# Performance work log

Hardware: AMD Instinct MI355X
Metric: run time of the kernel (lower is better)

## Reference

```python
import jax, jax.numpy as jnp
import numpy as np

EPS = 1e-6
NUM_HEADS = 24

def _rmsnorm(x, w):
    # x: [..., D], fp32 math as in FluxRMSNorm
    xf = x.astype(jnp.float32)
    inv = jax.lax.rsqrt(jnp.mean(xf * xf, axis=-1, keepdims=True) + EPS)
    return w * (xf * inv).astype(x.dtype)

def setup_inputs() -> dict:
    key = jax.random.key(0)
    ks = jax.random.split(key, 4)
    B, N, H = 1, 2048, 3072
    D = H // NUM_HEADS
    s_in = 1.0 / np.sqrt(H)
    return {
        "x": jax.random.normal(ks[0], (B, N, H), jnp.float32),
        "Wqkv": jax.random.normal(ks[1], (H, 3 * H), jnp.float32) * s_in,
        "b_qkv": jnp.zeros((3 * H,), jnp.float32),
        "Wproj": jax.random.normal(ks[2], (H, H), jnp.float32) * s_in,
        "q_norm_w": jnp.ones((D,), jnp.float32),
        "k_norm_w": jnp.ones((D,), jnp.float32),
    }

def reference(x, Wqkv, b_qkv, Wproj, q_norm_w, k_norm_w):
    B, N, hidden = x.shape
    nh = NUM_HEADS
    hd = hidden // nh
    scale = hd ** (-0.5)
    qkv = (x @ Wqkv + b_qkv).reshape(B, N, 3, nh, hd)
    q, k, v = qkv[:, :, 0], qkv[:, :, 1], qkv[:, :, 2]  # [B,N,nh,hd]
    q = _rmsnorm(q, q_norm_w)
    k = _rmsnorm(k, k_norm_w)
    # scores: [B,nh,N,N]
    scores = jnp.einsum('bqhd,bkhd->bhqk', q, k) * scale
    attn = jax.nn.softmax(scores, axis=-1)
    out = jnp.einsum('bhqk,bkhd->bqhd', attn, v).reshape(B, N, hidden)
    return out @ Wproj
```

## Files before the change

### kernel.cpp

```cpp
#include <hip/hip_runtime.h>
#include <hip/hip_bf16.h>

using bf16 = __hip_bfloat16;
typedef __attribute__((ext_vector_type(8))) short short8;
typedef __attribute__((ext_vector_type(4))) float f32x4;
typedef unsigned long long ull;

static constexpr int SEQ  = 2048;
static constexpr int HID  = 3072;
static constexpr int NH   = 24;
static constexpr int HD   = 128;
static constexpr int QKVN = 9216;

__device__ __forceinline__ f32x4 mfma_16x16x32(short8 a, short8 b, f32x4 c) {
  return __builtin_amdgcn_mfma_f32_16x16x32_bf16(a, b, c, 0, 0, 0);
}

#define GLOAD_LDS16(g, l) __builtin_amdgcn_global_load_lds(                 \
    (const __attribute__((address_space(1))) void*)(g),                    \
    (__attribute__((address_space(3))) void*)(l), 16, 0, 0)

typedef __attribute__((address_space(3))) const unsigned char lds_cchar;

__device__ __forceinline__ unsigned pack_bf16(float lo, float hi) {
  bf16 l = __float2bfloat16(lo), h = __float2bfloat16(hi);
  return (unsigned)*(unsigned short*)&l | ((unsigned)*(unsigned short*)&h << 16);
}

__global__ __launch_bounds__(256)
void cvt_f32_bf16_vec(const float* __restrict__ src, bf16* __restrict__ dst, int n4) {
  int i = blockIdx.x * 256 + threadIdx.x;
  if (i >= n4) return;
  float4 v = ((const float4*)src)[i];
  ushort4 o;
  bf16 t0 = __float2bfloat16(v.x); o.x = *(unsigned short*)&t0;
  bf16 t1 = __float2bfloat16(v.y); o.y = *(unsigned short*)&t1;
  bf16 t2 = __float2bfloat16(v.z); o.z = *(unsigned short*)&t2;
  bf16 t3 = __float2bfloat16(v.w); o.w = *(unsigned short*)&t3;
  ((ushort4*)dst)[i] = o;
}

__global__ __launch_bounds__(256)
void transpose_cvt64(const float* __restrict__ src, bf16* __restrict__ dst, int R, int C) {
  __shared__ float tile[32][65];
  const int c0 = blockIdx.x * 64, r0 = blockIdx.y * 32;
  const int lc = threadIdx.x & 63, lt = threadIdx.x >> 6;
  #pragma unroll
  for (int i = 0; i < 8; ++i)
    tile[lt + i * 4][lc] = src[(size_t)(r0 + lt + i * 4) * C + c0 + lc];
  __syncthreads();
  const int u = threadIdx.x & 15, dr = threadIdx.x >> 4;
  #pragma unroll
  for (int j = 0; j < 4; ++j) {
    const int cc = dr + j * 16;
    bf16 x0 = __float2bfloat16(tile[u * 2][cc]);
    bf16 x1 = __float2bfloat16(tile[u * 2 + 1][cc]);
    ushort2 o;
    o.x = *(unsigned short*)&x0; o.y = *(unsigned short*)&x1;
    *(ushort2*)&dst[(size_t)(c0 + cc) * R + r0 + u * 2] = o;
  }
}

template<int BIAS>
__global__ __launch_bounds__(768, 3)
void gemm12w(const bf16* __restrict__ A, const bf16* __restrict__ BT,
             const float* __restrict__ bias, bf16* __restrict__ Cout,
             int M, int N, int K) {
  __shared__ __align__(16) bf16 Asb[2][256 * 64];
  __shared__ __align__(16) bf16 Bsb[2][288 * 64];

  const int tid  = threadIdx.x;
  const int lane = tid & 63;
  const int wid  = tid >> 6;
  const int wm   = wid / 6;
  const int wn   = wid % 6;
  const int lr   = lane & 15;
  const int lg   = lane >> 4;

  const int xcd = blockIdx.x & 7;
  const int q   = blockIdx.x >> 3;
  const int bm  = (q & 7) * 256;
  const int bn  = (xcd * 4 + (q >> 3)) * 288;

  const int lrow = lane >> 3;
  const int csrc = ((lane & 7) ^ lrow) * 8;
  const bf16* Abase = A  + (size_t)(bm + lrow) * K + csrc;
  const bf16* Bbase = BT + (size_t)(bn + lrow) * K + csrc;

#define STG12(b, u, i) do {                                                       \
    const int L_ = wid + 12 * (i);                                                \
    if (L_ < 32)      GLOAD_LDS16(Abase + (size_t)(8 * L_) * K + (size_t)(u) * 64,\
                                  &Asb[b][L_ * 512]);                             \
    else if (L_ < 68) GLOAD_LDS16(Bbase + (size_t)(8 * (L_ - 32)) * K + (size_t)(u) * 64, \
                                  &Bsb[b][(L_ - 32) * 512]);                      \
  } while (0)
#define RA12(b, m, kk) (*(const short8*)(&Asb[b][(wm * 128 + (m) * 16 + lr) * 64 \
                          + ((((kk) * 4 + lg)) ^ (lr & 7)) * 8]))
#define RB12(b, n, kk) (*(const short8*)(&Bsb[b][(wn * 48 + (n) * 16 + lr) * 64 \
                          + ((((kk) * 4 + lg)) ^ (lr & 7)) * 8]))

  f32x4 acc[8][3] = {};
  const int NT = K >> 6;

  #pragma unroll
  for (int i = 0; i < 6; ++i) STG12(0, 0, i);

  for (int t = 0; t < NT; ++t) {
    const int c = t & 1, nc = c ^ 1;
    const bool pf = (t + 1) < NT;
    short8 a[4], b[3];

    asm volatile("s_waitcnt vmcnt(0)" ::: "memory");
    __builtin_amdgcn_s_barrier();

    if (pf) {
      STG12(nc, t + 1, 0); STG12(nc, t + 1, 1); STG12(nc, t + 1, 2);
      STG12(nc, t + 1, 3); STG12(nc, t + 1, 4); STG12(nc, t + 1, 5);
    }
    __builtin_amdgcn_sched_barrier(0);

    b[0] = RB12(c, 0, 0); b[1] = RB12(c, 1, 0); b[2] = RB12(c, 2, 0);
    a[0] = RA12(c, 0, 0); a[1] = RA12(c, 1, 0); a[2] = RA12(c, 2, 0); a[3] = RA12(c, 3, 0);
    #pragma unroll
    for (int n = 0; n < 3; ++n)
      #pragma unroll
      for (int m = 0; m < 4; ++m) acc[m][n] = mfma_16x16x32(a[m], b[n], acc[m][n]);

    a[0] = RA12(c, 4, 0); a[1] = RA12(c, 5, 0); a[2] = RA12(c, 6, 0); a[3] = RA12(c, 7, 0);
    #pragma unroll
    for (int n = 0; n < 3; ++n)
      #pragma unroll
      for (int m = 0; m < 4; ++m) acc[4 + m][n] = mfma_16x16x32(a[m], b[n], acc[4 + m][n]);

    b[0] = RB12(c, 0, 1); b[1] = RB12(c, 1, 1); b[2] = RB12(c, 2, 1);
    a[0] = RA12(c, 0, 1); a[1] = RA12(c, 1, 1); a[2] = RA12(c, 2, 1); a[3] = RA12(c, 3, 1);
    #pragma unroll
    for (int n = 0; n < 3; ++n)
      #pragma unroll
      for (int m = 0; m < 4; ++m) acc[m][n] = mfma_16x16x32(a[m], b[n], acc[m][n]);

    a[0] = RA12(c, 4, 1); a[1] = RA12(c, 5, 1); a[2] = RA12(c, 6, 1); a[3] = RA12(c, 7, 1);
    #pragma unroll
    for (int n = 0; n < 3; ++n)
      #pragma unroll
      for (int m = 0; m < 4; ++m) acc[4 + m][n] = mfma_16x16x32(a[m], b[n], acc[4 + m][n]);
  }
#undef STG12
#undef RA12
#undef RB12

  const int row0 = bm + wm * 128 + lg * 4;
  const int col0 = bn + wn * 48 + lr;
  #pragma unroll
  for (int n = 0; n < 3; ++n) {
    const int col = col0 + n * 16;
    const float bv = BIAS ? bias[col] : 0.0f;
    #pragma unroll
    for (int m = 0; m < 8; ++m)
      #pragma unroll
      for (int r = 0; r < 4; ++r)
        Cout[(size_t)(row0 + m * 16 + r) * N + col] = __float2bfloat16(acc[m][n][r] + bv);
  }
}

__global__ __launch_bounds__(512, 2)
void gemm8w(const bf16* __restrict__ A, const bf16* __restrict__ BT,
            float* __restrict__ Cout, int M, int N, int K) {
  __shared__ __align__(16) bf16 Asb[2][128 * 64];
  __shared__ __align__(16) bf16 Bsb[2][192 * 64];

  const int tid  = threadIdx.x;
  const int lane = tid & 63;
  const int wid  = tid >> 6;
  const int wm   = wid >> 2;
  const int wn   = wid & 3;
  const int lr   = lane & 15;
  const int lg   = lane >> 4;

  const int xcd = blockIdx.x & 7;
  const int q   = blockIdx.x >> 3;
  const int bm  = (q >> 1) * 128;
  const int bn  = (xcd * 2 + (q & 1)) * 192;

  const int lrow = lane >> 3;
  const int csrc = ((lane & 7) ^ lrow) * 8;
  const bf16* Abase = A  + (size_t)(bm + lrow) * K + csrc;
  const bf16* Bbase = BT + (size_t)(bn + lrow) * K + csrc;

#define STG8(b, u, i) do {                                                        \
    const int L_ = wid + 8 * (i);                                                 \
    if (L_ < 16)      GLOAD_LDS16(Abase + (size_t)(8 * L_) * K + (size_t)(u) * 64,\
                                  &Asb[b][L_ * 512]);                             \
    else              GLOAD_LDS16(Bbase + (size_t)(8 * (L_ - 16)) * K + (size_t)(u) * 64, \
                                  &Bsb[b][(L_ - 16) * 512]);                      \
  } while (0)
#define RA8(b, m, kk) (*(const short8*)(&Asb[b][(wm * 64 + (m) * 16 + lr) * 64 \
                          + ((((kk) * 4 + lg)) ^ (lr & 7)) * 8]))
#define RB8(b, n, kk) (*(const short8*)(&Bsb[b][(wn * 48 + (n) * 16 + lr) * 64 \
                          + ((((kk) * 4 + lg)) ^ (lr & 7)) * 8]))

  f32x4 acc[4][3] = {};
  const int NT = K >> 6;

  #pragma unroll
  for (int i = 0; i < 5; ++i) STG8(0, 0, i);

  for (int t = 0; t < NT; ++t) {
    const int c = t & 1, nc = c ^ 1;
    const bool pf = (t + 1) < NT;
    short8 a[4], b[3];

    asm volatile("s_waitcnt vmcnt(0)" ::: "memory");
    __builtin_amdgcn_s_barrier();

    if (pf) {
      STG8(nc, t + 1, 0); STG8(nc, t + 1, 1); STG8(nc, t + 1, 2);
      STG8(nc, t + 1, 3); STG8(nc, t + 1, 4);
    }
    __builtin_amdgcn_sched_barrier(0);

    b[0] = RB8(c, 0, 0); b[1] = RB8(c, 1, 0); b[2] = RB8(c, 2, 0);
    a[0] = RA8(c, 0, 0); a[1] = RA8(c, 1, 0); a[2] = RA8(c, 2, 0); a[3] = RA8(c, 3, 0);
    #pragma unroll
    for (int n = 0; n < 3; ++n)
      #pragma unroll
      for (int m = 0; m < 4; ++m) acc[m][n] = mfma_16x16x32(a[m], b[n], acc[m][n]);

    b[0] = RB8(c, 0, 1); b[1] = RB8(c, 1, 1); b[2] = RB8(c, 2, 1);
    a[0] = RA8(c, 0, 1); a[1] = RA8(c, 1, 1); a[2] = RA8(c, 2, 1); a[3] = RA8(c, 3, 1);
    #pragma unroll
    for (int n = 0; n < 3; ++n)
      #pragma unroll
      for (int m = 0; m < 4; ++m) acc[m][n] = mfma_16x16x32(a[m], b[n], acc[m][n]);
  }
#undef STG8
#undef RA8
#undef RB8

  const int row0 = bm + wm * 64 + lg * 4;
  const int col0 = bn + wn * 48 + lr;
  #pragma unroll
  for (int n = 0; n < 3; ++n) {
    const int col = col0 + n * 16;
    #pragma unroll
    for (int m = 0; m < 4; ++m)
      #pragma unroll
      for (int r = 0; r < 4; ++r)
        Cout[(size_t)(row0 + m * 16 + r) * N + col] = acc[m][n][r];
  }
}

__global__ __launch_bounds__(256)
void rmsnorm_qk(bf16* __restrict__ qkv, const float* __restrict__ qw,
                const float* __restrict__ kw) {
  const int row  = blockIdx.x * 4 + (threadIdx.x >> 6);
  const int lane = threadIdx.x & 63;
  const int token = row / 48;
  const int rem   = row - token * 48;
  const int which = rem / 24;
  const int head  = rem - which * 24;
  bf16* p = qkv + (long)token * QKVN + which * HID + head * HD;
  const float a = __bfloat162float(p[lane * 2]);
  const float b = __bfloat162float(p[lane * 2 + 1]);
  float ss = a * a + b * b;
  #pragma unroll
  for (int mask = 32; mask >= 1; mask >>= 1) ss += __shfl_xor(ss, mask);
  const float inv = rsqrtf(ss * (1.0f / 128.0f) + 1e-6f);
  const float* w = which ? kw : qw;
  p[lane * 2]     = __float2bfloat16(a * inv * w[lane * 2]);
  p[lane * 2 + 1] = __float2bfloat16(b * inv * w[lane * 2 + 1]);
}

__global__ __launch_bounds__(256, 3)
void attn_kernel(const bf16* __restrict__ qkv, bf16* __restrict__ ctx) {
  const int head = blockIdx.y;
  const int qb   = blockIdx.x;
  const int tid  = threadIdx.x;
  const int lane = tid & 63;
  const int wid  = tid >> 6;
  const int lr   = lane & 15;
  const int lg   = lane >> 4;

  __shared__ __align__(16) unsigned char Ksb[64 * 256];
  __shared__ __align__(16) unsigned char Vsb[128 * 128];
  __shared__ __align__(16) unsigned short Ps[4][16 * 72];

  const int qrow0 = qb * 64 + wid * 16;
  short8 qf[4];
  #pragma unroll
  for (int kt = 0; kt < 4; ++kt)
    qf[kt] = *(const short8*)(qkv + (long)(qrow0 + lr) * QKVN + head * HD + kt * 32 + lg * 8);

  f32x4 oacc[8] = {};
  float mrun = -1e30f, lsum = 0.0f;

  const float scale = 0.088388347648318447f;

  const int stok = tid >> 4;
  const int sdc  = tid & 15;

  short8 kreg[4], vreg[4];
  #pragma unroll
  for (int j = 0; j < 4; ++j) {
    const int tok = stok + (j & 1) * 16 + (j >> 1) * 32;
    kreg[j] = *(const short8*)(qkv + (long)tok * QKVN + HID     + head * HD + sdc * 8);
    vreg[j] = *(const short8*)(qkv + (long)tok * QKVN + 2 * HID + head * HD + sdc * 8);
  }

  for (int t = 0; t < SEQ / 64; ++t) {
    __syncthreads();
    #pragma unroll
    for (int j = 0; j < 4; ++j) {
      const int tok = stok + (j & 1) * 16 + (j >> 1) * 32;
      const int dc  = sdc;
      *(short8*)(Ksb + ((tok * 256 + dc * 16) ^ ((tok & 7) << 4))) = kreg[j];
      const int dg = dc >> 1, h = dc & 1, kg = tok >> 2, kr = tok & 3;
      const int pos = (kg & 8) | ((kg & 1) << 2) | ((kg >> 1) & 3);
      *(short8*)(Vsb + (dg * 16 + pos) * 128 + kr * 32 + h * 16) = vreg[j];
    }
    __syncthreads();

    if (t + 1 < SEQ / 64) {
      const int kv1 = (t + 1) * 64;
      #pragma unroll
      for (int j = 0; j < 4; ++j) {
        const int tok = kv1 + stok + (j & 1) * 16 + (j >> 1) * 32;
        kreg[j] = *(const short8*)(qkv + (long)tok * QKVN + HID     + head * HD + sdc * 8);
        vreg[j] = *(const short8*)(qkv + (long)tok * QKVN + 2 * HID + head * HD + sdc * 8);
      }
      __builtin_amdgcn_sched_barrier(0);
    }

    f32x4 st[4];
    __builtin_amdgcn_s_setprio(1);
    #pragma unroll
    for (int ct = 0; ct < 4; ++ct) {
      f32x4 a = {};
      #pragma unroll
      for (int kt = 0; kt < 4; ++kt) {
        short8 kb = *(const short8*)(Ksb +
            ((((ct * 16 + lr) * 256) + kt * 64 + lg * 16) ^ ((lr & 7) << 4)));
        a = mfma_16x16x32(kb, qf[kt], a);
      }
      st[ct] = a;
    }
    __builtin_amdgcn_s_setprio(0);

    float pm = st[0][0];
    #pragma unroll
    for (int ct = 0; ct < 4; ++ct)
      #pragma unroll
      for (int r = 0; r < 4; ++r) pm = fmaxf(pm, st[ct][r]);
    pm *= scale;
    pm = fmaxf(pm, __shfl_xor(pm, 16));
    pm = fmaxf(pm, __shfl_xor(pm, 32));

    if (!__all(pm <= mrun + 8.0f)) {
      const float mnew = fmaxf(mrun, pm);
      const float corr = __expf(mrun - mnew);
      mrun = mnew;
      lsum *= corr;
      #pragma unroll
      for (int r = 0; r < 4; ++r) {
        const float cr = __shfl(corr, lg * 4 + r);
        #pragma unroll
        for (int dt = 0; dt < 8; ++dt) oacc[dt][r] *= cr;
      }
    }

    float ps = 0.0f;
    #pragma unroll
    for (int ct = 0; ct < 4; ++ct) {
      const float p0 = __expf(st[ct][0] * scale - mrun);
      const float p1 = __expf(st[ct][1] * scale - mrun);
      const float p2 = __expf(st[ct][2] * scale - mrun);
      const float p3 = __expf(st[ct][3] * scale - mrun);
      ps += (p0 + p1) + (p2 + p3);
      uint2 w;
      w.x = pack_bf16(p0, p1);
      w.y = pack_bf16(p2, p3);
      *(uint2*)&Ps[wid][lr * 72 + ct * 16 + lg * 4] = w;
    }
    lsum += ps;

    short8 pa[2];
    #pragma unroll
    for (int kt = 0; kt < 2; ++kt)
      pa[kt] = *(const short8*)&Ps[wid][lr * 72 + kt * 32 + lg * 8];

    lds_cchar* vb0 = (lds_cchar*)Vsb + lane * 8;
    __builtin_amdgcn_s_setprio(1);
    #pragma unroll
    for (int dt = 0; dt < 8; ++dt) {
      lds_cchar* pd = vb0 + dt * 2048;
      ull r0, r1, r2, r3;
      asm volatile("ds_read_b64_tr_b16 %0, %1 offset:0"    : "=v"(r0) : "v"(pd));
      asm volatile("ds_read_b64_tr_b16 %0, %1 offset:512"  : "=v"(r1) : "v"(pd));
      asm volatile("ds_read_b64_tr_b16 %0, %1 offset:1024" : "=v"(r2) : "v"(pd));
      asm volatile("ds_read_b64_tr_b16 %0, %1 offset:1536" : "=v"(r3) : "v"(pd));
      asm volatile("s_waitcnt lgkmcnt(0)" ::: "memory");
      __builtin_amdgcn_sched_barrier(0);
      short8 vb_0, vb_1;
      ((ull*)&vb_0)[0] = r0; ((ull*)&vb_0)[1] = r1;
      ((ull*)&vb_1)[0] = r2; ((ull*)&vb_1)[1] = r3;
      oacc[dt] = mfma_16x16x32(pa[0], vb_0, oacc[dt]);
      oacc[dt] = mfma_16x16x32(pa[1], vb_1, oacc[dt]);
    }
    __builtin_amdgcn_s_setprio(0);
  }

  lsum += __shfl_xor(lsum, 16);
  lsum += __shfl_xor(lsum, 32);
  const float invl = 1.0f / lsum;
  #pragma unroll
  for (int r = 0; r < 4; ++r) {
    const float inv = __shfl(invl, lg * 4 + r);
    const long tok = qrow0 + lg * 4 + r;
    #pragma unroll
    for (int dt = 0; dt < 8; ++dt)
      ctx[tok * HID + head * HD + dt * 16 + lr] = __float2bfloat16(oacc[dt][r] * inv);
  }
}

extern "C" void kernel_launch(void* const* d_in, const int* in_sizes, int n_in,
                              void* d_out, int out_size, void* d_ws, size_t ws_size,
                              hipStream_t stream) {
  (void)in_sizes; (void)n_in; (void)out_size; (void)ws_size;
  const float* x     = (const float*)d_in[0];
  const float* Wqkv  = (const float*)d_in[1];
  const float* bqkv  = (const float*)d_in[2];
  const float* Wproj = (const float*)d_in[3];
  const float* qw    = (const float*)d_in[4];
  const float* kw    = (const float*)d_in[5];

  char* ws = (char*)d_ws;
  bf16* xb     = (bf16*)ws;
  bf16* WqkvT  = (bf16*)(ws + 12582912);
  bf16* WprojT = (bf16*)(ws + 69206016);
  bf16* qkv    = (bf16*)(ws + 88080384);
  bf16* ctx    = xb;

  cvt_f32_bf16_vec<<<(SEQ * HID / 4 + 255) / 256, 256, 0, stream>>>(x, xb, SEQ * HID / 4);
  transpose_cvt64<<<dim3(QKVN / 64, HID / 32), 256, 0, stream>>>(Wqkv, WqkvT, HID, QKVN);
  transpose_cvt64<<<dim3(HID / 64, HID / 32), 256, 0, stream>>>(Wproj, WprojT, HID, HID);

  gemm12w<1><<<256, 768, 0, stream>>>(xb, WqkvT, bqkv, qkv, SEQ, QKVN, HID);

  rmsnorm_qk<<<SEQ * 48 / 4, 256, 0, stream>>>(qkv, qw, kw);

  attn_kernel<<<dim3(SEQ / 64, NH), 256, 0, stream>>>(qkv, ctx);

  gemm8w<<<256, 512, 0, stream>>>(ctx, WprojT, (float*)d_out, SEQ, HID, HID);
}
```

Measured before the change: 322.9 us.

## Double-buffer V transposed reads in attention and retile projection GEMM to 4 waves

The attention PV loop now issues the transposed LDS reads for the next head-dim tile before waiting on the current one, using lgkmcnt(4) so LDS latency overlaps the MFMAs instead of draining fully each step. Separately, the output projection GEMM moves from 8-wave 128x192 tiles to 4-wave 128x96 tiles over 512 blocks, giving more blocks and smaller LDS per block. The new tiling changes the XCD block mapping and the reuse of A tiles, and the software pipeline holds more registers live.

```diff
diff --git a/kernel.cpp b/kernel.cpp
--- a/kernel.cpp
+++ b/kernel.cpp
@@ -163,47 +163,47 @@
   }
 }
 
-__global__ __launch_bounds__(512, 2)
-void gemm8w(const bf16* __restrict__ A, const bf16* __restrict__ BT,
+__global__ __launch_bounds__(256, 2)
+void gemm4w(const bf16* __restrict__ A, const bf16* __restrict__ BT,
             float* __restrict__ Cout, int M, int N, int K) {
   __shared__ __align__(16) bf16 Asb[2][128 * 64];
-  __shared__ __align__(16) bf16 Bsb[2][192 * 64];
+  __shared__ __align__(16) bf16 Bsb[2][96 * 64];
 
   const int tid  = threadIdx.x;
   const int lane = tid & 63;
   const int wid  = tid >> 6;
-  const int wm   = wid >> 2;
-  const int wn   = wid & 3;
+  const int wm   = wid >> 1;
+  const int wn   = wid & 1;
   const int lr   = lane & 15;
   const int lg   = lane >> 4;
 
   const int xcd = blockIdx.x & 7;
   const int q   = blockIdx.x >> 3;
-  const int bm  = (q >> 1) * 128;
-  const int bn  = (xcd * 2 + (q & 1)) * 192;
+  const int bm  = (q & 15) * 128;
+  const int bn  = (xcd * 4 + (q >> 4)) * 96;
 
   const int lrow = lane >> 3;
   const int csrc = ((lane & 7) ^ lrow) * 8;
   const bf16* Abase = A  + (size_t)(bm + lrow) * K + csrc;
   const bf16* Bbase = BT + (size_t)(bn + lrow) * K + csrc;
 
-#define STG8(b, u, i) do {                                                        \
-    const int L_ = wid + 8 * (i);                                                 \
+#define STG4(b, u, i) do {                                                        \
+    const int L_ = wid + 4 * (i);                                                 \
     if (L_ < 16)      GLOAD_LDS16(Abase + (size_t)(8 * L_) * K + (size_t)(u) * 64,\
                                   &Asb[b][L_ * 512]);                             \
-    else              GLOAD_LDS16(Bbase + (size_t)(8 * (L_ - 16)) * K + (size_t)(u) * 64, \
+    else if (L_ < 28) GLOAD_LDS16(Bbase + (size_t)(8 * (L_ - 16)) * K + (size_t)(u) * 64, \
                                   &Bsb[b][(L_ - 16) * 512]);                      \
   } while (0)
-#define RA8(b, m, kk) (*(const short8*)(&Asb[b][(wm * 64 + (m) * 16 + lr) * 64 \
+#define RA4(b, m, kk) (*(const short8*)(&Asb[b][(wm * 64 + (m) * 16 + lr) * 64 \
                           + ((((kk) * 4 + lg)) ^ (lr & 7)) * 8]))
-#define RB8(b, n, kk) (*(const short8*)(&Bsb[b][(wn * 48 + (n) * 16 + lr) * 64 \
+#define RB4(b, n, kk) (*(const short8*)(&Bsb[b][(wn * 48 + (n) * 16 + lr) * 64 \
                           + ((((kk) * 4 + lg)) ^ (lr & 7)) * 8]))
 
   f32x4 acc[4][3] = {};
   const int NT = K >> 6;
 
   #pragma unroll
-  for (int i = 0; i < 5; ++i) STG8(0, 0, i);
+  for (int i = 0; i < 7; ++i) STG4(0, 0, i);
 
   for (int t = 0; t < NT; ++t) {
     const int c = t & 1, nc = c ^ 1;
@@ -214,28 +214,28 @@
     __builtin_amdgcn_s_barrier();
 
     if (pf) {
-      STG8(nc, t + 1, 0); STG8(nc, t + 1, 1); STG8(nc, t + 1, 2);
-      STG8(nc, t + 1, 3); STG8(nc, t + 1, 4);
+      STG4(nc, t + 1, 0); STG4(nc, t + 1, 1); STG4(nc, t + 1, 2); STG4(nc, t + 1, 3);
+      STG4(nc, t + 1, 4); STG4(nc, t + 1, 5); STG4(nc, t + 1, 6);
     }
     __builtin_amdgcn_sched_barrier(0);
 
-    b[0] = RB8(c, 0, 0); b[1] = RB8(c, 1, 0); b[2] = RB8(c, 2, 0);
-    a[0] = RA8(c, 0, 0); a[1] = RA8(c, 1, 0); a[2] = RA8(c, 2, 0); a[3] = RA8(c, 3, 0);
+    b[0] = RB4(c, 0, 0); b[1] = RB4(c, 1, 0); b[2] = RB4(c, 2, 0);
+    a[0] = RA4(c, 0, 0); a[1] = RA4(c, 1, 0); a[2] = RA4(c, 2, 0); a[3] = RA4(c, 3, 0);
     #pragma unroll
     for (int n = 0; n < 3; ++n)
       #pragma unroll
       for (int m = 0; m < 4; ++m) acc[m][n] = mfma_16x16x32(a[m], b[n], acc[m][n]);
 
-    b[0] = RB8(c, 0, 1); b[1] = RB8(c, 1, 1); b[2] = RB8(c, 2, 1);
-    a[0] = RA8(c, 0, 1); a[1] = RA8(c, 1, 1); a[2] = RA8(c, 2, 1); a[3] = RA8(c, 3, 1);
+    b[0] = RB4(c, 0, 1); b[1] = RB4(c, 1, 1); b[2] = RB4(c, 2, 1);
+    a[0] = RA4(c, 0, 1); a[1] = RA4(c, 1, 1); a[2] = RA4(c, 2, 1); a[3] = RA4(c, 3, 1);
     #pragma unroll
     for (int n = 0; n < 3; ++n)
       #pragma unroll
       for (int m = 0; m < 4; ++m) acc[m][n] = mfma_16x16x32(a[m], b[n], acc[m][n]);
   }
-#undef STG8
-#undef RA8
-#undef RB8
+#undef STG4
+#undef RA4
+#undef RB4
 
   const int row0 = bm + wm * 64 + lg * 4;
   const int col0 = bn + wn * 48 + lr;
@@ -307,6 +307,21 @@
     vreg[j] = *(const short8*)(qkv + (long)tok * QKVN + 2 * HID + head * HD + sdc * 8);
   }
 
+#define TRISSUE(S, dtv) {                                                         \
+    lds_cchar* pd_ = vb0 + (dtv) * 2048;                                          \
+    asm volatile("ds_read_b64_tr_b16 %0, %1 offset:0"    : "=v"(S##0) : "v"(pd_));\
+    asm volatile("ds_read_b64_tr_b16 %0, %1 offset:512"  : "=v"(S##1) : "v"(pd_));\
+    asm volatile("ds_read_b64_tr_b16 %0, %1 offset:1024" : "=v"(S##2) : "v"(pd_));\
+    asm volatile("ds_read_b64_tr_b16 %0, %1 offset:1536" : "=v"(S##3) : "v"(pd_));}
+#define TRMFMA(S, dtv) {                                                          \
+    short8 v0_, v1_;                                                              \
+    ((ull*)&v0_)[0] = S##0; ((ull*)&v0_)[1] = S##1;                               \
+    ((ull*)&v1_)[0] = S##2; ((ull*)&v1_)[1] = S##3;                               \
+    oacc[dtv] = mfma_16x16x32(pa[0], v0_, oacc[dtv]);                             \
+    oacc[dtv] = mfma_16x16x32(pa[1], v1_, oacc[dtv]); }
+#define TRWAIT4 asm volatile("s_waitcnt lgkmcnt(4)" ::: "memory"); \
+                __builtin_amdgcn_sched_barrier(0);
+
   for (int t = 0; t < SEQ / 64; ++t) {
     __syncthreads();
     #pragma unroll
@@ -384,30 +399,30 @@
     lsum += ps;
 
     short8 pa[2];
-    #pragma unroll
-    for (int kt = 0; kt < 2; ++kt)
-      pa[kt] = *(const short8*)&Ps[wid][lr * 72 + kt * 32 + lg * 8];
+    pa[0] = *(const short8*)&Ps[wid][lr * 72 + lg * 8];
+    pa[1] = *(const short8*)&Ps[wid][lr * 72 + 32 + lg * 8];
+    __builtin_amdgcn_sched_barrier(0);
 
     lds_cchar* vb0 = (lds_cchar*)Vsb + lane * 8;
+    ull x0, x1, x2, x3, y0, y1, y2, y3;
     __builtin_amdgcn_s_setprio(1);
-    #pragma unroll
-    for (int dt = 0; dt < 8; ++dt) {
-      lds_cchar* pd = vb0 + dt * 2048;
-      ull r0, r1, r2, r3;
-      asm volatile("ds_read_b64_tr_b16 %0, %1 offset:0"    : "=v"(r0) : "v"(pd));
-      asm volatile("ds_read_b64_tr_b16 %0, %1 offset:512"  : "=v"(r1) : "v"(pd));
-      asm volatile("ds_read_b64_tr_b16 %0, %1 offset:1024" : "=v"(r2) : "v"(pd));
-      asm volatile("ds_read_b64_tr_b16 %0, %1 offset:1536" : "=v"(r3) : "v"(pd));
-      asm volatile("s_waitcnt lgkmcnt(0)" ::: "memory");
-      __builtin_amdgcn_sched_barrier(0);
-      short8 vb_0, vb_1;
-      ((ull*)&vb_0)[0] = r0; ((ull*)&vb_0)[1] = r1;
-      ((ull*)&vb_1)[0] = r2; ((ull*)&vb_1)[1] = r3;
-      oacc[dt] = mfma_16x16x32(pa[0], vb_0, oacc[dt]);
-      oacc[dt] = mfma_16x16x32(pa[1], vb_1, oacc[dt]);
-    }
+    TRISSUE(x, 0)
+    TRISSUE(y, 1)
+    TRWAIT4  TRMFMA(x, 0)  TRISSUE(x, 2)
+    TRWAIT4  TRMFMA(y, 1)  TRISSUE(y, 3)
+    TRWAIT4  TRMFMA(x, 2)  TRISSUE(x, 4)
+    TRWAIT4  TRMFMA(y, 3)  TRISSUE(y, 5)
+    TRWAIT4  TRMFMA(x, 4)  TRISSUE(x, 6)
+    TRWAIT4  TRMFMA(y, 5)  TRISSUE(y, 7)
+    TRWAIT4  TRMFMA(x, 6)
+    asm volatile("s_waitcnt lgkmcnt(0)" ::: "memory");
+    __builtin_amdgcn_sched_barrier(0);
+    TRMFMA(y, 7)
     __builtin_amdgcn_s_setprio(0);
   }
+#undef TRISSUE
+#undef TRMFMA
+#undef TRWAIT4
 
   lsum += __shfl_xor(lsum, 16);
   lsum += __shfl_xor(lsum, 32);
@@ -450,5 +465,5 @@
 
   attn_kernel<<<dim3(SEQ / 64, NH), 256, 0, stream>>>(qkv, ctx);
 
-  gemm8w<<<256, 512, 0, stream>>>(ctx, WprojT, (float*)d_out, SEQ, HID, HID);
-}
+  gemm4w<<<512, 256, 0, stream>>>(ctx, WprojT, (float*)d_out, SEQ, HID, HID);
+}
```

Result: faster. 313.8 us (-2.8%).
